# Kernel optimization log

Hardware: AMD Instinct MI355X
Metric: run time of the kernel (lower is better)

The kernel has to match this reference:

```python
import jax, jax.numpy as jnp
import numpy as np

B, K, G = 1024, 32, 1024
NUM_NODES, NUM_EDGES = 200000, 1000000
NODE_DIM, EDGE_DIM, TIME_DIM = 128, 128, 100
NEG_INF = -1.0e10


def setup_inputs() -> dict:
    key = jax.random.key(0)
    ks = jax.random.split(key, 12)
    node_ids = jax.random.randint(ks[0], (B,), 0, NUM_NODES)
    node_interact_times = jax.random.uniform(ks[1], (B,), jnp.float32) * 1000.0
    neighbor_node_ids = jax.random.randint(ks[2], (B, K), 0, NUM_NODES)
    neighbor_edge_ids = jax.random.randint(ks[3], (B, K), 0, NUM_EDGES)
    neighbor_times = jax.random.uniform(ks[4], (B, K), jnp.float32) * 1000.0
    time_gap_neighbor_node_ids = jax.random.randint(ks[5], (B, G), 0, NUM_NODES)
    node_raw_features = jax.random.normal(ks[6], (NUM_NODES, NODE_DIM), jnp.float32)
    edge_raw_features = jax.random.normal(ks[7], (NUM_EDGES, EDGE_DIM), jnp.float32)
    # TimeEncoder: cos(t * w + b), w fixed to 1/10^linspace(0,9,T), b=0
    time_w = (1.0 / (10.0 ** jnp.linspace(0.0, 9.0, TIME_DIM))).astype(jnp.float32)
    time_b = jnp.zeros((TIME_DIM,), jnp.float32)
    sc = 0.05
    W_edge = jax.random.normal(ks[8], (EDGE_DIM + TIME_DIM, EDGE_DIM), jnp.float32) * sc
    b_edge = jnp.zeros((EDGE_DIM,), jnp.float32)
    w_final = jax.random.normal(ks[9], (K,), jnp.float32) * sc
    b_final = jnp.zeros((1,), jnp.float32)
    W_node = jax.random.normal(ks[10], (EDGE_DIM + NODE_DIM, NODE_DIM), jnp.float32) * sc
    b_node = jnp.zeros((NODE_DIM,), jnp.float32)
    return dict(node_ids=node_ids, node_interact_times=node_interact_times,
                neighbor_node_ids=neighbor_node_ids, neighbor_edge_ids=neighbor_edge_ids,
                neighbor_times=neighbor_times,
                time_gap_neighbor_node_ids=time_gap_neighbor_node_ids,
                node_raw_features=node_raw_features, edge_raw_features=edge_raw_features,
                time_w=time_w, time_b=time_b, W_edge=W_edge, b_edge=b_edge,
                w_final=w_final, b_final=b_final, W_node=W_node, b_node=b_node)


def reference(node_ids, node_interact_times, neighbor_node_ids, neighbor_edge_ids,
              neighbor_times, time_gap_neighbor_node_ids, node_raw_features,
              edge_raw_features, time_w, time_b, W_edge, b_edge, w_final, b_final,
              W_node, b_node):
    # --- edge branch: gather + time-encode + edge MLP + pool over neighbors ---
    dt = node_interact_times[:, None] - neighbor_times              # [B,K]
    time_feats = jnp.cos(dt[..., None] * time_w + time_b)            # [B,K,T]
    time_feats = jnp.where((neighbor_node_ids == 0)[..., None], 0.0, time_feats)
    edge_feats = edge_raw_features[neighbor_edge_ids]                # [B,K,E]
    combined = jnp.concatenate([edge_feats, time_feats], axis=-1)    # [B,K,E+T]
    combined = combined @ W_edge + b_edge                            # [B,K,E]
    pooled = jnp.einsum('bke,k->be', combined, w_final) + b_final    # edge_final_mlp over K
    # --- node branch: time-gap neighbor gather + masked-softmax mean ---
    gfeat = node_raw_features[time_gap_neighbor_node_ids]            # [B,G,N]
    mask = jnp.where(time_gap_neighbor_node_ids > 0, 1.0, NEG_INF)   # [B,G]
    scores = jax.nn.softmax(mask, axis=1)
    agg = jnp.mean(gfeat * scores[..., None], axis=1)                # [B,N]
    out_node = agg + node_raw_features[node_ids]                     # [B,N]
    # --- final projection ---
    emb = jnp.concatenate([pooled, out_node], axis=-1) @ W_node + b_node  # [B,N]
    return emb
```

## Files before the change

### kernel.cpp

```cpp
#include <hip/hip_runtime.h>
#include <hip/hip_bf16.h>

#define B_  1024
#define K_  32
#define G_  1024
#define TD_ 100
#define ED_ 128
#define ND_ 128

__device__ __forceinline__ float bf_lo(unsigned u){ union{unsigned q; float f;} c; c.q = u << 16; return c.f; }
__device__ __forceinline__ float bf_hi(unsigned u){ union{unsigned q; float f;} c; c.q = u & 0xFFFF0000u; return c.f; }

template<typename T> __device__ __forceinline__ float ldf(const T* p);
template<> __device__ __forceinline__ float ldf<float>(const float* p){ return *p; }
template<> __device__ __forceinline__ float ldf<__hip_bfloat16>(const __hip_bfloat16* p){
    unsigned short s = *(const unsigned short*)p;
    union{unsigned q; float f;} c; c.q = ((unsigned)s) << 16; return c.f;
}

template<typename T> __device__ __forceinline__ float2 ld2(const T* p);
template<> __device__ __forceinline__ float2 ld2<float>(const float* p){ return *(const float2*)p; }
template<> __device__ __forceinline__ float2 ld2<__hip_bfloat16>(const __hip_bfloat16* p){
    unsigned u = *(const unsigned*)p;
    float2 r; r.x = bf_lo(u); r.y = bf_hi(u); return r;
}

template<typename T> __device__ __forceinline__ T stf(float v);
template<> __device__ __forceinline__ float stf<float>(float v){ return v; }
template<> __device__ __forceinline__ __hip_bfloat16 stf<__hip_bfloat16>(float v){ return __float2bfloat16(v); }

template<typename T>
__global__ __launch_bounds__(256, 4) void fused_tgat(
    const int* __restrict__ node_ids,
    const T*   __restrict__ nit,
    const int* __restrict__ nbr_ids,
    const int* __restrict__ nbr_eids,
    const T*   __restrict__ nbr_t,
    const int* __restrict__ tg_ids,
    const T*   __restrict__ nraw,
    const T*   __restrict__ eraw,
    const T*   __restrict__ tw,
    const T*   __restrict__ tb,
    const T*   __restrict__ We,
    const T*   __restrict__ be,
    const T*   __restrict__ wf,
    const T*   __restrict__ bfin,
    const T*   __restrict__ Wn,
    const T*   __restrict__ bn,
    T*         __restrict__ out)
{
    constexpr bool BF16 = (sizeof(T) == 2);
    {
        unsigned w0 = *(const unsigned*)tw;
        bool data_is_f32 = (w0 == 0x3F800000u);
        if (data_is_f32 == BF16) return;
    }
    const int b = blockIdx.x;
    const int t = threadIdx.x;

    __shared__ int   s_ids[G_];
    __shared__ float s_dt[K_], s_wf[K_], s_wfm[K_];
    __shared__ int   s_eid[K_];
    __shared__ float s_cat[ED_ + TD_];
    __shared__ float s_pooled[ED_];
    __shared__ float s_on[ND_];
    __shared__ float s_red[2 * ND_];
    __shared__ int   s_cnt[4];

    {
        const int4* p = (const int4*)(tg_ids + (size_t)b * G_);
        int4 v = p[t];
        *(int4*)&s_ids[4 * t] = v;
    }
    if (t < K_) {
        float ntk = ldf(nbr_t + (size_t)b * K_ + t);
        float itb = ldf(nit + b);
        float wfk = ldf(wf + t);
        int   nid = nbr_ids[(size_t)b * K_ + t];
        s_dt[t]  = itb - ntk;
        s_wf[t]  = wfk;
        s_wfm[t] = (nid == 0) ? 0.0f : wfk;
        s_eid[t] = nbr_eids[(size_t)b * K_ + t];
    }
    __syncthreads();

    if (t < ED_) {
        float acc = 0.0f;
        #pragma unroll 8
        for (int k = 0; k < K_; ++k)
            acc = fmaf(s_wf[k], ldf(eraw + (size_t)s_eid[k] * ED_ + t), acc);
        s_cat[t] = acc;
    } else if (t < ED_ + TD_) {
        int tt = t - ED_;
        float wv = ldf(tw + tt);
        float bv = ldf(tb + tt);
        float acc = 0.0f;
        #pragma unroll 4
        for (int k = 0; k < K_; ++k)
            acc = fmaf(s_wfm[k], cosf(fmaf(s_dt[k], wv, bv)), acc);
        s_cat[t] = acc;
    }
    __syncthreads();

    if (t < ED_) {
        float swf = 0.0f;
        #pragma unroll
        for (int k = 0; k < K_; ++k) swf += s_wf[k];
        float acc = fmaf(swf, ldf(be + t), ldf(bfin));
        #pragma unroll 4
        for (int j = 0; j < ED_ + TD_; ++j)
            acc = fmaf(s_cat[j], ldf(We + (size_t)j * ED_ + t), acc);
        s_pooled[t] = acc;
    }

    const int lane = t & 63;
    const int grp  = t >> 6;
    const int d0   = 2 * lane;
    float a0 = 0.0f, a1 = 0.0f;
    int cnt = 0;
    #pragma unroll 4
    for (int g = grp; g < G_; g += 4) {
        int id = s_ids[g];
        if (id > 0) {
            ++cnt;
            float2 v = ld2(nraw + (size_t)id * ND_ + d0);
            a0 += v.x; a1 += v.y;
        }
    }
    if (grp >= 2) *(float2*)&s_red[(grp - 2) * ND_ + d0] = make_float2(a0, a1);
    if (lane == 0) s_cnt[grp] = cnt;
    __syncthreads();
    if (grp < 2) {
        float2 v = *(const float2*)&s_red[grp * ND_ + d0];
        a0 += v.x; a1 += v.y;
    }
    __syncthreads();
    if (grp == 1) *(float2*)&s_red[d0] = make_float2(a0, a1);
    __syncthreads();
    if (grp == 0) {
        float2 v = *(const float2*)&s_red[d0];
        a0 += v.x; a1 += v.y;
        int nv = s_cnt[0] + s_cnt[1] + s_cnt[2] + s_cnt[3];
        float scale = (nv > 0) ? 1.0f / (1024.0f * (float)nv) : 0.0f;
        int nid = node_ids[b];
        float2 nr = ld2(nraw + (size_t)nid * ND_ + d0);
        s_on[d0]     = fmaf(a0, scale, nr.x);
        s_on[d0 + 1] = fmaf(a1, scale, nr.y);
    }
    __syncthreads();

    float facc = 0.0f;
    if (t < ND_) {
        #pragma unroll 4
        for (int j = 0; j < ED_; ++j)
            facc = fmaf(s_pooled[j], ldf(Wn + (size_t)j * ND_ + t), facc);
    } else {
        int e = t - ND_;
        #pragma unroll 4
        for (int j = 0; j < ND_; ++j)
            facc = fmaf(s_on[j], ldf(Wn + (size_t)(ED_ + j) * ND_ + e), facc);
        s_red[e] = facc;
    }
    __syncthreads();
    if (t < ND_) {
        float r = facc + s_red[t] + ldf(bn + t);
        out[(size_t)b * ND_ + t] = stf<T>(r);
    }
}

extern "C" void kernel_launch(void* const* d_in, const int* in_sizes, int n_in,
                              void* d_out, int out_size, void* d_ws, size_t ws_size,
                              hipStream_t stream) {
    (void)in_sizes; (void)n_in; (void)out_size; (void)d_ws; (void)ws_size;
    dim3 grid(B_), block(256);
    fused_tgat<float><<<grid, block, 0, stream>>>(
        (const int*)d_in[0], (const float*)d_in[1], (const int*)d_in[2],
        (const int*)d_in[3], (const float*)d_in[4], (const int*)d_in[5],
        (const float*)d_in[6], (const float*)d_in[7], (const float*)d_in[8],
        (const float*)d_in[9], (const float*)d_in[10], (const float*)d_in[11],
        (const float*)d_in[12], (const float*)d_in[13], (const float*)d_in[14],
        (const float*)d_in[15], (float*)d_out);
    fused_tgat<__hip_bfloat16><<<grid, block, 0, stream>>>(
        (const int*)d_in[0], (const __hip_bfloat16*)d_in[1], (const int*)d_in[2],
        (const int*)d_in[3], (const __hip_bfloat16*)d_in[4], (const int*)d_in[5],
        (const __hip_bfloat16*)d_in[6], (const __hip_bfloat16*)d_in[7],
        (const __hip_bfloat16*)d_in[8], (const __hip_bfloat16*)d_in[9],
        (const __hip_bfloat16*)d_in[10], (const __hip_bfloat16*)d_in[11],
        (const __hip_bfloat16*)d_in[12], (const __hip_bfloat16*)d_in[13],
        (const __hip_bfloat16*)d_in[14], (const __hip_bfloat16*)d_in[15],
        (__hip_bfloat16*)d_out);
}
```

Measured before the change: 748.9 us.

## Rebalance work across waves, vectorize gather, and skip redundant dtype launch

The edge branch (edge gather, time encoding, edge MLP) now runs on one wave with two outputs per lane. The other three waves, plus the rest of wave 0, split the 1024 time-gap neighbors unevenly with float4 loads and branchless masking, so that gather overlaps the edge work. Reduction uses a lane shuffle and a single shared-memory pass instead of two staged barriers. The host now looks at input sizes to launch only the matching dtype instantiation, which saves a redundant launch. The cost is that masked-out rows are still loaded, and the edge MLP is serialized on a single wave.

```diff
diff --git a/kernel.cpp b/kernel.cpp
--- a/kernel.cpp
+++ b/kernel.cpp
@@ -23,6 +23,13 @@
 template<> __device__ __forceinline__ float2 ld2<__hip_bfloat16>(const __hip_bfloat16* p){
     unsigned u = *(const unsigned*)p;
     float2 r; r.x = bf_lo(u); r.y = bf_hi(u); return r;
+}
+
+template<typename T> __device__ __forceinline__ float4 ld4(const T* p);
+template<> __device__ __forceinline__ float4 ld4<float>(const float* p){ return *(const float4*)p; }
+template<> __device__ __forceinline__ float4 ld4<__hip_bfloat16>(const __hip_bfloat16* p){
+    uint2 u = *(const uint2*)p;
+    return make_float4(bf_lo(u.x), bf_hi(u.x), bf_lo(u.y), bf_hi(u.y));
 }
 
 template<typename T> __device__ __forceinline__ T stf(float v);
@@ -55,16 +62,21 @@
         bool data_is_f32 = (w0 == 0x3F800000u);
         if (data_is_f32 == BF16) return;
     }
-    const int b = blockIdx.x;
-    const int t = threadIdx.x;
-
-    __shared__ int   s_ids[G_];
+    const int b    = blockIdx.x;
+    const int t    = threadIdx.x;
+    const int lane = t & 63;
+    const int grp  = t >> 6;
+    const int half = lane >> 5;
+    const int l5   = lane & 31;
+    const int c0   = 4 * l5;
+
+    __shared__ __align__(16) int   s_ids[G_];
     __shared__ float s_dt[K_], s_wf[K_], s_wfm[K_];
     __shared__ int   s_eid[K_];
     __shared__ float s_cat[ED_ + TD_];
     __shared__ float s_pooled[ED_];
-    __shared__ float s_on[ND_];
-    __shared__ float s_red[2 * ND_];
+    __shared__ __align__(16) float s_on[ND_];
+    __shared__ __align__(16) float s_red[4 * ND_];
     __shared__ int   s_cnt[4];
 
     {
@@ -72,80 +84,101 @@
         int4 v = p[t];
         *(int4*)&s_ids[4 * t] = v;
     }
-    if (t < K_) {
-        float ntk = ldf(nbr_t + (size_t)b * K_ + t);
-        float itb = ldf(nit + b);
-        float wfk = ldf(wf + t);
-        int   nid = nbr_ids[(size_t)b * K_ + t];
-        s_dt[t]  = itb - ntk;
-        s_wf[t]  = wfk;
-        s_wfm[t] = (nid == 0) ? 0.0f : wfk;
-        s_eid[t] = nbr_eids[(size_t)b * K_ + t];
-    }
-    __syncthreads();
-
-    if (t < ED_) {
-        float acc = 0.0f;
-        #pragma unroll 8
-        for (int k = 0; k < K_; ++k)
-            acc = fmaf(s_wf[k], ldf(eraw + (size_t)s_eid[k] * ED_ + t), acc);
-        s_cat[t] = acc;
-    } else if (t < ED_ + TD_) {
-        int tt = t - ED_;
-        float wv = ldf(tw + tt);
-        float bv = ldf(tb + tt);
-        float acc = 0.0f;
-        #pragma unroll 4
-        for (int k = 0; k < K_; ++k)
-            acc = fmaf(s_wfm[k], cosf(fmaf(s_dt[k], wv, bv)), acc);
-        s_cat[t] = acc;
-    }
-    __syncthreads();
-
-    if (t < ED_) {
+    __syncthreads();
+
+    if (grp == 0) {
+        if (lane < 32) {
+            float ntk = ldf(nbr_t + (size_t)b * K_ + lane);
+            float itb = ldf(nit + b);
+            float wfk = ldf(wf + lane);
+            int   nid = nbr_ids[(size_t)b * K_ + lane];
+            s_dt[lane]  = itb - ntk;
+            s_wf[lane]  = wfk;
+            s_wfm[lane] = (nid == 0) ? 0.0f : wfk;
+            s_eid[lane] = nbr_eids[(size_t)b * K_ + lane];
+        }
+        __builtin_amdgcn_wave_barrier();
+
+        float wv0 = ldf(tw + lane);
+        float bv0 = ldf(tb + lane);
+        const int tt1 = (lane < TD_ - 64) ? (lane + 64) : 0;
+        float wv1 = ldf(tw + tt1);
+        float bv1 = ldf(tb + tt1);
+        float e0 = 0.0f, e1 = 0.0f, ta0 = 0.0f, ta1 = 0.0f;
+        #pragma unroll 4
+        for (int k = 0; k < K_; ++k) {
+            float wfk = s_wf[k];
+            float2 ev = ld2(eraw + (size_t)s_eid[k] * ED_ + 2 * lane);
+            e0 = fmaf(wfk, ev.x, e0);
+            e1 = fmaf(wfk, ev.y, e1);
+            float dtk = s_dt[k];
+            float wmk = s_wfm[k];
+            ta0 = fmaf(wmk, cosf(fmaf(dtk, wv0, bv0)), ta0);
+            ta1 = fmaf(wmk, cosf(fmaf(dtk, wv1, bv1)), ta1);
+        }
+        s_cat[2 * lane]     = e0;
+        s_cat[2 * lane + 1] = e1;
+        s_cat[ED_ + lane]   = ta0;
+        if (lane < TD_ - 64) s_cat[ED_ + 64 + lane] = ta1;
+        __builtin_amdgcn_wave_barrier();
+
         float swf = 0.0f;
         #pragma unroll
         for (int k = 0; k < K_; ++k) swf += s_wf[k];
-        float acc = fmaf(swf, ldf(be + t), ldf(bfin));
-        #pragma unroll 4
-        for (int j = 0; j < ED_ + TD_; ++j)
-            acc = fmaf(s_cat[j], ldf(We + (size_t)j * ED_ + t), acc);
-        s_pooled[t] = acc;
-    }
-
-    const int lane = t & 63;
-    const int grp  = t >> 6;
-    const int d0   = 2 * lane;
-    float a0 = 0.0f, a1 = 0.0f;
+        float  bfv = ldf(bfin);
+        float2 bev = ld2(be + 2 * lane);
+        float pa = fmaf(swf, bev.x, bfv);
+        float pb = fmaf(swf, bev.y, bfv);
+        #pragma unroll 4
+        for (int j = 0; j < ED_ + TD_; ++j) {
+            float  cj = s_cat[j];
+            float2 wv = ld2(We + (size_t)j * ED_ + 2 * lane);
+            pa = fmaf(cj, wv.x, pa);
+            pb = fmaf(cj, wv.y, pb);
+        }
+        s_pooled[2 * lane]     = pa;
+        s_pooled[2 * lane + 1] = pb;
+    }
+
+    const int beg = (grp == 0) ? 0  : (64 + (grp - 1) * 320);
+    const int end = (grp == 0) ? 64 : (beg + 320);
+    float a0 = 0.0f, a1 = 0.0f, a2 = 0.0f, a3 = 0.0f;
     int cnt = 0;
     #pragma unroll 4
-    for (int g = grp; g < G_; g += 4) {
-        int id = s_ids[g];
-        if (id > 0) {
-            ++cnt;
-            float2 v = ld2(nraw + (size_t)id * ND_ + d0);
-            a0 += v.x; a1 += v.y;
-        }
-    }
-    if (grp >= 2) *(float2*)&s_red[(grp - 2) * ND_ + d0] = make_float2(a0, a1);
+    for (int g = beg + half; g < end; g += 2) {
+        int   id = s_ids[g];
+        int   v  = (id > 0);
+        float m  = (float)v;
+        cnt += v;
+        float4 r = ld4(nraw + (size_t)id * ND_ + c0);
+        a0 = fmaf(m, r.x, a0);
+        a1 = fmaf(m, r.y, a1);
+        a2 = fmaf(m, r.z, a2);
+        a3 = fmaf(m, r.w, a3);
+    }
+    a0 += __shfl_xor(a0, 32);
+    a1 += __shfl_xor(a1, 32);
+    a2 += __shfl_xor(a2, 32);
+    a3 += __shfl_xor(a3, 32);
+    cnt += __shfl_xor(cnt, 32);
+    if (half == 0) *(float4*)&s_red[grp * ND_ + c0] = make_float4(a0, a1, a2, a3);
     if (lane == 0) s_cnt[grp] = cnt;
     __syncthreads();
-    if (grp < 2) {
-        float2 v = *(const float2*)&s_red[grp * ND_ + d0];
-        a0 += v.x; a1 += v.y;
-    }
-    __syncthreads();
-    if (grp == 1) *(float2*)&s_red[d0] = make_float2(a0, a1);
-    __syncthreads();
-    if (grp == 0) {
-        float2 v = *(const float2*)&s_red[d0];
-        a0 += v.x; a1 += v.y;
+
+    if (t < 32) {
+        float4 s = make_float4(0.0f, 0.0f, 0.0f, 0.0f);
+        #pragma unroll
+        for (int w = 0; w < 4; ++w) {
+            float4 v = *(const float4*)&s_red[w * ND_ + 4 * t];
+            s.x += v.x; s.y += v.y; s.z += v.z; s.w += v.w;
+        }
         int nv = s_cnt[0] + s_cnt[1] + s_cnt[2] + s_cnt[3];
         float scale = (nv > 0) ? 1.0f / (1024.0f * (float)nv) : 0.0f;
         int nid = node_ids[b];
-        float2 nr = ld2(nraw + (size_t)nid * ND_ + d0);
-        s_on[d0]     = fmaf(a0, scale, nr.x);
-        s_on[d0 + 1] = fmaf(a1, scale, nr.y);
+        float4 nr = ld4(nraw + (size_t)nid * ND_ + 4 * t);
+        *(float4*)&s_on[4 * t] = make_float4(
+            fmaf(s.x, scale, nr.x), fmaf(s.y, scale, nr.y),
+            fmaf(s.z, scale, nr.z), fmaf(s.w, scale, nr.w));
     }
     __syncthreads();
 
@@ -155,7 +188,7 @@
         for (int j = 0; j < ED_; ++j)
             facc = fmaf(s_pooled[j], ldf(Wn + (size_t)j * ND_ + t), facc);
     } else {
-        int e = t - ND_;
+        const int e = t - ND_;
         #pragma unroll 4
         for (int j = 0; j < ND_; ++j)
             facc = fmaf(s_on[j], ldf(Wn + (size_t)(ED_ + j) * ND_ + e), facc);
@@ -171,22 +204,35 @@
 extern "C" void kernel_launch(void* const* d_in, const int* in_sizes, int n_in,
                               void* d_out, int out_size, void* d_ws, size_t ws_size,
                               hipStream_t stream) {
-    (void)in_sizes; (void)n_in; (void)out_size; (void)d_ws; (void)ws_size;
+    (void)out_size; (void)d_ws; (void)ws_size;
     dim3 grid(B_), block(256);
-    fused_tgat<float><<<grid, block, 0, stream>>>(
-        (const int*)d_in[0], (const float*)d_in[1], (const int*)d_in[2],
-        (const int*)d_in[3], (const float*)d_in[4], (const int*)d_in[5],
-        (const float*)d_in[6], (const float*)d_in[7], (const float*)d_in[8],
-        (const float*)d_in[9], (const float*)d_in[10], (const float*)d_in[11],
-        (const float*)d_in[12], (const float*)d_in[13], (const float*)d_in[14],
-        (const float*)d_in[15], (float*)d_out);
-    fused_tgat<__hip_bfloat16><<<grid, block, 0, stream>>>(
-        (const int*)d_in[0], (const __hip_bfloat16*)d_in[1], (const int*)d_in[2],
-        (const int*)d_in[3], (const __hip_bfloat16*)d_in[4], (const int*)d_in[5],
-        (const __hip_bfloat16*)d_in[6], (const __hip_bfloat16*)d_in[7],
-        (const __hip_bfloat16*)d_in[8], (const __hip_bfloat16*)d_in[9],
-        (const __hip_bfloat16*)d_in[10], (const __hip_bfloat16*)d_in[11],
-        (const __hip_bfloat16*)d_in[12], (const __hip_bfloat16*)d_in[13],
-        (const __hip_bfloat16*)d_in[14], (const __hip_bfloat16*)d_in[15],
-        (__hip_bfloat16*)d_out);
-}
+
+    int dt = 0;
+    if (in_sizes && n_in >= 16) {
+        if (in_sizes[1] == (int)(B_ * sizeof(float)) ||
+            in_sizes[6] == (int)(200000 * ND_ * sizeof(float)))   dt = 1;
+        else if (in_sizes[1] == (int)(B_ * sizeof(short)) ||
+                 in_sizes[6] == (int)(200000 * ND_ * sizeof(short))) dt = 2;
+    }
+
+    if (dt != 2) {
+        fused_tgat<float><<<grid, block, 0, stream>>>(
+            (const int*)d_in[0], (const float*)d_in[1], (const int*)d_in[2],
+            (const int*)d_in[3], (const float*)d_in[4], (const int*)d_in[5],
+            (const float*)d_in[6], (const float*)d_in[7], (const float*)d_in[8],
+            (const float*)d_in[9], (const float*)d_in[10], (const float*)d_in[11],
+            (const float*)d_in[12], (const float*)d_in[13], (const float*)d_in[14],
+            (const float*)d_in[15], (float*)d_out);
+    }
+    if (dt != 1) {
+        fused_tgat<__hip_bfloat16><<<grid, block, 0, stream>>>(
+            (const int*)d_in[0], (const __hip_bfloat16*)d_in[1], (const int*)d_in[2],
+            (const int*)d_in[3], (const __hip_bfloat16*)d_in[4], (const int*)d_in[5],
+            (const __hip_bfloat16*)d_in[6], (const __hip_bfloat16*)d_in[7],
+            (const __hip_bfloat16*)d_in[8], (const __hip_bfloat16*)d_in[9],
+            (const __hip_bfloat16*)d_in[10], (const __hip_bfloat16*)d_in[11],
+            (const __hip_bfloat16*)d_in[12], (const __hip_bfloat16*)d_in[13],
+            (const __hip_bfloat16*)d_in[14], (const __hip_bfloat16*)d_in[15],
+            (__hip_bfloat16*)d_out);
+    }
+}
```

New measurement: 693.7 us. 7.4% less time.
